# Kernel tuning notes

Hardware: AMD Instinct MI355X
Metric: run time of the kernel (lower is better)

The kernel has to match this reference:

```python
import jax, jax.numpy as jnp
import numpy as np

RADIUS = 3  # module init_kwargs radius=3 -> diameter 7, 49 taps
EPS_NORM = 1e-12   # F.normalize eps
EPS_KSUM = 1e-7    # kernel-sum clamp used in JBU.forward


def setup_inputs() -> dict:
    key = jax.random.key(0)
    k1, k2 = jax.random.split(key)
    B, SC, SH, SW = 2, 384, 112, 112
    GC, GH, GW = 3, 224, 224
    source = jax.random.normal(k1, (B, SC, SH, SW), dtype=jnp.float32)
    guidance = jax.random.uniform(k2, (B, GC, GH, GW), dtype=jnp.float32)
    sigma_spatial = jnp.asarray(4.0, dtype=jnp.float32)   # nn.Parameter init
    sigma_range = jnp.asarray(0.25, dtype=jnp.float32)    # nn.Parameter init
    return {"source": source, "guidance": guidance,
            "sigma_spatial": sigma_spatial, "sigma_range": sigma_range}


def reference(source, guidance, sigma_spatial, sigma_range):
    radius = RADIUS
    d = 2 * radius + 1
    B, SC, SH, SW = source.shape
    GB, GC, GH, GW = guidance.shape
    ss = jnp.abs(sigma_spatial)
    sr = jnp.abs(sigma_range)

    # bilinear upsample source to guidance resolution (align_corners=False,
    # half-pixel centers == jax.image.resize 'bilinear')
    hr = jax.image.resize(source, (B, SC, GH, GW), method='bilinear')

    # channel-wise L2 normalize guidance (F.normalize dim=1)
    g = guidance / jnp.maximum(
        jnp.linalg.norm(guidance, axis=1, keepdims=True), EPS_NORM)

    # reflect-pad both by radius on H, W
    pad = ((0, 0), (0, 0), (radius, radius), (radius, radius))
    gp = jnp.pad(g, pad, mode='reflect')
    sp = jnp.pad(hr, pad, mode='reflect')

    # spatial Gaussian kernel over offsets, flattened to P = d*d
    rr = jnp.arange(d, dtype=source.dtype) - radius
    yy, xx = jnp.meshgrid(rr, rr, indexing='ij')
    ks = jnp.exp(-(xx ** 2 + yy ** 2) / (2.0 * ss ** 2)).reshape(d * d)  # [P]

    # range kernel: per-pixel dot of each neighborhood pixel with center
    # (Unfold patch order = row-major over kernel offsets)
    patches = jnp.stack(
        [gp[:, :, i:i + GH, j:j + GW] for i in range(d) for j in range(d)],
        axis=2)  # [B, GC, P, GH, GW]
    rk = 2.0 - jnp.einsum('bcphw,bchw->bphw', patches, g)  # GC > 1 branch
    rk = jnp.exp(-rk ** 2 / (2.0 * sr ** 2))

    # combine and normalize per pixel
    ck = rk * ks[None, :, None, None]                       # [B, P, GH, GW]
    ck = ck / jnp.maximum(ck.sum(axis=1, keepdims=True), EPS_KSUM)

    # adaptive conv: out[b,c,h,w] = sum_p ck[b,p,h,w] * sp[b,c,h+i,w+j]
    # accumulate over the 49 static offsets (no giant [B,SC,P,GH,GW] tensor)
    out = jnp.zeros((B, SC, GH, GW), dtype=source.dtype)
    p = 0
    for i in range(d):
        for j in range(d):
            out = out + ck[:, p][:, None] * sp[:, :, i:i + GH, j:j + GW]
            p += 1
    return out
```

## Files before the change

kernel.cpp:

```cpp
#include <hip/hip_runtime.h>
#include <math.h>

#define BB   2
#define SC   384
#define SH   112
#define SW   112
#define GH   224
#define GW   224
#define HWs  (SH*SW)
#define HWg  (GH*GW)
#define GT   22
#define NCB  2
#define CPB  (SC/NCB)

typedef float f32x2 __attribute__((ext_vector_type(2)));

__device__ __forceinline__ int reflect224(int v){
    v = v < 0 ? -v : v;
    v = v > 223 ? 446 - v : v;
    return v;
}

__launch_bounds__(256, 2)
__global__ void jbu_kernel(const float* __restrict__ src,
                           const float* __restrict__ gdn,
                           const float* __restrict__ sigs,
                           const float* __restrict__ sigr,
                           float* __restrict__ out)
{
    __shared__ float gtile[GT*GT*3];
    __shared__ float slab[25*256];
    __shared__ float invs_sh[256];

    const int bx = blockIdx.x;
    const int cb = bx / 392;
    const int r  = bx - cb*392;
    const int b  = r / 196;
    const int t  = r - b*196;
    const int th = t / 14, tw = t - th*14;
    const int h0 = th*16, w0 = tw*16;

    const int tid = threadIdx.x;

    const float ssv  = fabsf(sigs[0]);
    const float srv  = fabsf(sigr[0]);
    const float i2ss = 0.5f/(ssv*ssv);
    const float i2sr = 0.5f/(srv*srv);

    #pragma unroll
    for (int k=0;k<25;k++) slab[k*256+tid] = 0.f;

    const float* gb = gdn + (size_t)b*3*HWg;
    for (int idx = tid; idx < GT*GT; idx += 256){
        int ty = idx / GT, tx = idx - ty*GT;
        int y = reflect224(h0 - 3 + ty);
        int x = reflect224(w0 - 3 + tx);
        float g0 = gb[y*GW + x];
        float g1 = gb[HWg   + y*GW + x];
        float g2 = gb[2*HWg + y*GW + x];
        float nrm = sqrtf(g0*g0 + g1*g1 + g2*g2);
        float inv = 1.0f / fmaxf(nrm, 1e-12f);
        gtile[idx*3+0] = g0*inv;
        gtile[idx*3+1] = g1*inv;
        gtile[idx*3+2] = g2*inv;
    }
    __syncthreads();

    const int hh = tid >> 4, ww = tid & 15;
    const int h = h0 + hh, w = w0 + ww;
    const float c0 = gtile[((hh+3)*GT + (ww+3))*3 + 0];
    const float c1 = gtile[((hh+3)*GT + (ww+3))*3 + 1];
    const float c2 = gtile[((hh+3)*GT + (ww+3))*3 + 2];

    float wc0a[7]; int dc0a[7];
    #pragma unroll
    for (int j=0;j<7;j++){
        int xr = reflect224(w + j - 3);
        int a  = xr >> 1;
        int cs0 = a - 1 + (xr & 1);
        wc0a[j] = (xr & 1) ? 0.75f : 0.25f;
        dc0a[j] = cs0 - ((w>>1) - 2);
    }

    float sum = 0.f;
    #pragma unroll
    for (int i=0;i<7;i++){
        int yr = reflect224(h + i - 3);
        int a  = yr >> 1;
        int rs0 = a - 1 + (yr & 1);
        float wr0 = (yr & 1) ? 0.75f : 0.25f;
        int dr0 = rs0 - ((h>>1) - 2);
        const float* grow = &gtile[((hh+i)*GT + ww)*3];
        float di2 = (float)((i-3)*(i-3));
        #pragma unroll
        for (int j=0;j<7;j++){
            float dot = c0*grow[j*3+0] + c1*grow[j*3+1] + c2*grow[j*3+2];
            float t2  = 2.0f - dot;
            float dj2 = (float)((j-3)*(j-3));
            float ck  = __expf(-(t2*t2*i2sr + (di2+dj2)*i2ss));
            sum += ck;
            float p0 = ck*wr0, p1 = ck - p0;
            float wc0 = wc0a[j];
            float q00 = p0*wc0, q01 = p0 - q00;
            float q10 = p1*wc0, q11 = p1 - q10;
            int base = (dr0*5 + dc0a[j])*256 + tid;
            slab[base        ] += q00;
            slab[base +   256] += q01;
            slab[base + 5*256] += q10;
            slab[base + 6*256] += q11;
        }
    }
    invs_sh[tid] = 1.0f / fmaxf(sum, 1e-7f);
    __syncthreads();

    const int wid  = tid >> 6, lane = tid & 63;
    const int wm   = lane >> 3, wn = lane & 7;
    const int m    = th*8 + wm, n = tw*8 + wn;

    float wf[4][25];
    #pragma unroll
    for (int q=0;q<4;q++){
        int e = q>>1, f = q&1;
        int px = (2*wm+e)*16 + (2*wn+f);
        float inv = invs_sh[px];
        #pragma unroll
        for (int k=0;k<25;k++){
            float v_ = slab[k*256+px]*inv;
            asm volatile("" : "+v"(v_));
            wf[q][k] = v_;
        }
    }

    int voff[25];
    #pragma unroll
    for (int dr=0;dr<5;dr++){
        int sr_ = m - 2 + dr; sr_ = sr_ < 0 ? 0 : (sr_ > SH-1 ? SH-1 : sr_);
        #pragma unroll
        for (int dc=0;dc<5;dc++){
            int sc_ = n - 2 + dc; sc_ = sc_ < 0 ? 0 : (sc_ > SW-1 ? SW-1 : sc_);
            voff[dr*5+dc] = (sr_*SW + sc_)*4;
        }
    }
    const int ooffB = ((2*m)*GW + 2*n)*4;

    const int wid_u = __builtin_amdgcn_readfirstlane(wid);

    for (int it = 0; it < CPB/4; ++it){
        int c = cb*CPB + wid_u + it*4;
        const char* sb = (const char*)(src + (size_t)(b*SC + c)*HWs);
        float v[25];
        #pragma unroll
        for (int k=0;k<25;k++) v[k] = *(const float*)(sb + voff[k]);
        float a0=0.f, a1=0.f, a2=0.f, a3=0.f;
        #pragma unroll
        for (int k=0;k<25;k++){
            a0 += wf[0][k]*v[k];
            a1 += wf[1][k]*v[k];
            a2 += wf[2][k]*v[k];
            a3 += wf[3][k]*v[k];
        }
        char* ob = (char*)(out + (size_t)(b*SC + c)*HWg) + ooffB;
        f32x2 r0 = {a0, a1};
        f32x2 r1 = {a2, a3};
        __builtin_nontemporal_store(r0, (f32x2*)ob);
        __builtin_nontemporal_store(r1, (f32x2*)(ob + GW*4));
    }
}

extern "C" void kernel_launch(void* const* d_in, const int* in_sizes, int n_in,
                              void* d_out, int out_size, void* d_ws, size_t ws_size,
                              hipStream_t stream) {
    (void)in_sizes; (void)n_in; (void)d_ws; (void)ws_size; (void)out_size;
    const float* src  = (const float*)d_in[0];
    const float* gdn  = (const float*)d_in[1];
    const float* sigs = (const float*)d_in[2];
    const float* sigr = (const float*)d_in[3];
    float* out = (float*)d_out;

    dim3 grid(NCB * BB * 196);
    dim3 block(256);
    jbu_kernel<<<grid, block, 0, stream>>>(src, gdn, sigs, sigr, out);
}
```

Baseline: 338.5 us.

## Stage source tiles into LDS via async global_load_lds with double buffering

The per-channel gather of the 5x5 low-res neighbourhood is replaced by a cooperative 12x12 tile load straight into LDS using global_load_lds, double-buffered per wave and prefetched two iterations ahead with manual vmcnt waits. Each lane then reads its 25 taps from LDS instead of issuing 25 scattered global loads. The slab layout is also permuted so the weight read-back pattern has fewer bank conflicts. The cost is extra LDS space and hand-tuned waitcnt counts, which are fragile and could break correctness if the counts are wrong.

```diff
diff --git a/kernel.cpp b/kernel.cpp
--- a/kernel.cpp
+++ b/kernel.cpp
@@ -1,5 +1,6 @@
 #include <hip/hip_runtime.h>
 #include <math.h>
+#include <stdint.h>
 
 #define BB   2
 #define SC   384
@@ -12,13 +13,21 @@
 #define GT   22
 #define NCB  2
 #define CPB  (SC/NCB)
+#define NIT  (CPB/4)
 
 typedef float f32x2 __attribute__((ext_vector_type(2)));
+typedef __attribute__((address_space(3))) uint32_t lds_u32_t;
+typedef const __attribute__((address_space(1))) uint32_t glb_u32_t;
 
 __device__ __forceinline__ int reflect224(int v){
     v = v < 0 ? -v : v;
     v = v > 223 ? 446 - v : v;
     return v;
+}
+
+__device__ __forceinline__ int slabcol(int t){
+    int wm = t >> 5, e = (t >> 4) & 1, wn = (t >> 1) & 7, f = t & 1;
+    return (e << 7) | (f << 6) | (wm << 3) | wn;
 }
 
 __launch_bounds__(256, 2)
@@ -31,6 +40,7 @@
     __shared__ float gtile[GT*GT*3];
     __shared__ float slab[25*256];
     __shared__ float invs_sh[256];
+    __shared__ float lds_stage[4][2][192];
 
     const int bx = blockIdx.x;
     const int cb = bx / 392;
@@ -47,8 +57,9 @@
     const float i2ss = 0.5f/(ssv*ssv);
     const float i2sr = 0.5f/(srv*srv);
 
-    #pragma unroll
-    for (int k=0;k<25;k++) slab[k*256+tid] = 0.f;
+    const int mycol = slabcol(tid);
+    #pragma unroll
+    for (int k=0;k<25;k++) slab[k*256+mycol] = 0.f;
 
     const float* gb = gdn + (size_t)b*3*HWg;
     for (int idx = tid; idx < GT*GT; idx += 256){
@@ -103,7 +114,7 @@
             float wc0 = wc0a[j];
             float q00 = p0*wc0, q01 = p0 - q00;
             float q10 = p1*wc0, q11 = p1 - q10;
-            int base = (dr0*5 + dc0a[j])*256 + tid;
+            int base = (dr0*5 + dc0a[j])*256 + mycol;
             slab[base        ] += q00;
             slab[base +   256] += q01;
             slab[base + 5*256] += q10;
@@ -120,51 +131,85 @@
     float wf[4][25];
     #pragma unroll
     for (int q=0;q<4;q++){
-        int e = q>>1, f = q&1;
-        int px = (2*wm+e)*16 + (2*wn+f);
-        float inv = invs_sh[px];
+        const int e = q>>1, f = q&1;
+        const int px  = (2*wm+e)*16 + (2*wn+f);
+        const int col = (e<<7) | (f<<6) | (wm<<3) | wn;
+        const float inv = invs_sh[px];
+        volatile const float* vs = &slab[col];
         #pragma unroll
         for (int k=0;k<25;k++){
-            float v_ = slab[k*256+px]*inv;
+            float v_ = vs[k*256]*inv;
             asm volatile("" : "+v"(v_));
             wf[q][k] = v_;
         }
     }
 
-    int voff[25];
-    #pragma unroll
-    for (int dr=0;dr<5;dr++){
-        int sr_ = m - 2 + dr; sr_ = sr_ < 0 ? 0 : (sr_ > SH-1 ? SH-1 : sr_);
-        #pragma unroll
-        for (int dc=0;dc<5;dc++){
-            int sc_ = n - 2 + dc; sc_ = sc_ < 0 ? 0 : (sc_ > SW-1 ? SW-1 : sc_);
-            voff[dr*5+dc] = (sr_*SW + sc_)*4;
-        }
-    }
+    int soff[3];
+    #pragma unroll
+    for (int k2=0;k2<3;k2++){
+        int l = k2*64 + lane; if (l > 143) l = 143;
+        int rr_ = th*8 - 2 + l/12;
+        int cc_ = tw*8 - 2 + l%12;
+        rr_ = rr_ < 0 ? 0 : (rr_ > SH-1 ? SH-1 : rr_);
+        cc_ = cc_ < 0 ? 0 : (cc_ > SW-1 ? SW-1 : cc_);
+        soff[k2] = (rr_*SW + cc_)*4;
+    }
+
     const int ooffB = ((2*m)*GW + 2*n)*4;
-
     const int wid_u = __builtin_amdgcn_readfirstlane(wid);
-
-    for (int it = 0; it < CPB/4; ++it){
-        int c = cb*CPB + wid_u + it*4;
-        const char* sb = (const char*)(src + (size_t)(b*SC + c)*HWs);
-        float v[25];
-        #pragma unroll
-        for (int k=0;k<25;k++) v[k] = *(const float*)(sb + voff[k]);
-        float a0=0.f, a1=0.f, a2=0.f, a3=0.f;
-        #pragma unroll
-        for (int k=0;k<25;k++){
-            a0 += wf[0][k]*v[k];
-            a1 += wf[1][k]*v[k];
-            a2 += wf[2][k]*v[k];
-            a3 += wf[3][k]*v[k];
-        }
-        char* ob = (char*)(out + (size_t)(b*SC + c)*HWg) + ooffB;
-        f32x2 r0 = {a0, a1};
-        f32x2 r1 = {a2, a3};
-        __builtin_nontemporal_store(r0, (f32x2*)ob);
-        __builtin_nontemporal_store(r1, (f32x2*)(ob + GW*4));
-    }
+    const char* sp0 = (const char*)(src + (size_t)(b*SC + cb*CPB + wid_u)*HWs);
+    char*       op0 = (char*)(out + (size_t)(b*SC + cb*CPB + wid_u)*HWg) + ooffB;
+    float* buf0 = &lds_stage[wid_u][0][0];
+    float* buf1 = &lds_stage[wid_u][1][0];
+
+#define STAGE(BUFP, ITC) do { \
+        const char* _g = sp0 + (size_t)(ITC)*(4*HWs*4); \
+        lds_u32_t* _l = (lds_u32_t*)(BUFP); \
+        __builtin_amdgcn_global_load_lds((glb_u32_t*)(_g + soff[0]), _l      , 4, 0, 0); \
+        __builtin_amdgcn_global_load_lds((glb_u32_t*)(_g + soff[1]), _l +  64, 4, 0, 0); \
+        __builtin_amdgcn_global_load_lds((glb_u32_t*)(_g + soff[2]), _l + 128, 4, 0, 0); \
+    } while(0)
+
+#define ITER(IT, VM, CBUF, DO_PF) do { \
+        asm volatile("s_waitcnt vmcnt(" #VM ")" ::: "memory"); \
+        __builtin_amdgcn_sched_barrier(0); \
+        const float* _bp = (CBUF) + wm*12 + wn; \
+        float vv[25]; \
+        _Pragma("unroll") \
+        for (int dr=0;dr<5;dr++){ \
+            _Pragma("unroll") \
+            for (int dc=0;dc<5;dc++) vv[dr*5+dc] = _bp[dr*12+dc]; \
+        } \
+        asm volatile("s_waitcnt lgkmcnt(0)" ::: "memory"); \
+        __builtin_amdgcn_sched_barrier(0); \
+        if (DO_PF) STAGE(CBUF, (IT)+2); \
+        float a0=0.f,a1=0.f,a2=0.f,a3=0.f; \
+        _Pragma("unroll") \
+        for (int k=0;k<25;k++){ \
+            a0 += wf[0][k]*vv[k]; \
+            a1 += wf[1][k]*vv[k]; \
+            a2 += wf[2][k]*vv[k]; \
+            a3 += wf[3][k]*vv[k]; \
+        } \
+        char* _ob = op0 + (size_t)(IT)*(4*HWg*4); \
+        f32x2 _r0 = {a0,a1}, _r1 = {a2,a3}; \
+        __builtin_nontemporal_store(_r0, (f32x2*)_ob); \
+        __builtin_nontemporal_store(_r1, (f32x2*)(_ob + GW*4)); \
+    } while(0)
+
+    STAGE(buf0, 0);
+    STAGE(buf1, 1);
+    ITER(0, 3, buf0, true);
+    ITER(1, 5, buf1, true);
+    for (int it2 = 2; it2 < NIT-2; it2 += 2){
+        ITER(it2,   7, buf0, true);
+        ITER(it2+1, 7, buf1, true);
+    }
+    ITER(NIT-2, 7, buf0, false);
+    ITER(NIT-1, 4, buf1, false);
+
+#undef ITER
+#undef STAGE
 }
 
 extern "C" void kernel_launch(void* const* d_in, const int* in_sizes, int n_in,
```

Result: faster. 274.3 us (-19.0%).
